# Optimization experiments

Hardware: AMD Instinct MI355X
Metric: run time of the kernel (lower is better)

Reference implementation:

```python
import jax, jax.numpy as jnp
import numpy as np
from jax import lax

E = 192      # hidden size
NH = 6       # attention heads
L = 6        # mixer blocks (permutation length)
CO = 256     # merging output channels
KH, KW = 7, 11   # locality window
LOCAL = (False, False, True, True, True, True)
B, H, W = 64, 8, 64


def skew(x, pad_value):
    # shift every row one step right, turning columns into diagonals (torch skew)
    rest = x.shape[:-2]
    Hd, Wd = x.shape[-2], x.shape[-1]
    x = jnp.pad(x, [(0, 0)] * (x.ndim - 1) + [(0, Hd)], constant_values=pad_value)
    x = x.reshape(*rest, -1)[..., : Hd * (Hd + Wd - 1)]
    x = x.reshape(*rest, Hd, Hd + Wd - 1)
    end = (Hd + Wd - 1) - (Wd // 2) + (Wd % 2 - 1)
    return x[..., Wd // 2 : end]


def make_mask(h, w, kh, kw):
    # boolean [h*w, h*w]; True inside the local window (torch: True = NOT allowed)
    m = jnp.ones((h, w, kh, kw), dtype=bool)
    m = m.transpose(0, 2, 1, 3)        # [h, kh, w, kw]
    m = skew(m, 0)                     # [h, kh, w, w]
    m = m.transpose(2, 3, 0, 1)        # [w, w, h, kh]
    m = skew(m, 0)                     # [w, w, h, h]
    m = m.transpose(2, 0, 3, 1)        # [h, w, h, w]
    return m.reshape(h * w, h * w)


def layernorm(x, g, b, eps=1e-5):
    mu = jnp.mean(x, axis=-1, keepdims=True)
    var = jnp.mean((x - mu) ** 2, axis=-1, keepdims=True)
    return (x - mu) / jnp.sqrt(var + eps) * g + b


def mha(x, mask, wi, bi, wo, bo, nh):
    # torch nn.MultiheadAttention (batch_first, self-attn, inference)
    b, s, e = x.shape
    hd = e // nh
    qkv = x @ wi.T + bi                                   # [b, s, 3e]
    q, k, v = jnp.split(qkv, 3, axis=-1)
    to_heads = lambda t: t.reshape(b, s, nh, hd).transpose(0, 2, 1, 3)
    q, k, v = to_heads(q), to_heads(k), to_heads(v)
    scores = jnp.einsum('bhqd,bhkd->bhqk', q, k) / jnp.sqrt(jnp.asarray(hd, x.dtype))
    if mask is not None:
        scores = jnp.where(mask, -jnp.inf, scores)
    attn = jax.nn.softmax(scores, axis=-1)
    out = jnp.einsum('bhqk,bhkd->bhqd', attn, v)
    out = out.transpose(0, 2, 1, 3).reshape(b, s, e)
    return out @ wo.T + bo


def mixer_block(x, mask, wi, bi, wo, bo, g1, b1, g2, b2, wm1, bm1, wm2, bm2):
    x = layernorm(x, g1, b1)
    x = mha(x, mask, wi, bi, wo, bo, NH) + x
    x = layernorm(x, g2, b2)
    h = jax.nn.relu(x @ wm1.T + bm1)
    return h @ wm2.T + bm2 + x


def fvtr_stage(image, in_w, in_b, out_w, out_b, ln1_g, ln1_b, ln2_g, ln2_b,
               w1, b1, w2, b2, conv_w, conv_b, mln_g, mln_b):
    bsz, c, h, w = image.shape
    x = jnp.swapaxes(image, -1, -3).reshape(bsz, w * h, c)   # [B, W*H, C]
    mask = make_mask(h, w, KH, KW)
    for i, loc in enumerate(LOCAL):
        x = mixer_block(x, mask if loc else None,
                        in_w[i], in_b[i], out_w[i], out_b[i],
                        ln1_g[i], ln1_b[i], ln2_g[i], ln2_b[i],
                        w1[i], b1[i], w2[i], b2[i])
    x = jnp.swapaxes(x.reshape(bsz, w, h, c), -1, -3)        # [B, C, H, W]
    # MergingBlock: conv (3,1) stride (2,1) pad (1,0) + channel LayerNorm
    y = lax.conv_general_dilated(x, conv_w, window_strides=(2, 1),
                                 padding=((1, 1), (0, 0)),
                                 dimension_numbers=('NCHW', 'OIHW', 'NCHW'))
    y = y + conv_b[None, :, None, None]
    y = jnp.moveaxis(y, 1, -1)
    y = layernorm(y, mln_g, mln_b)
    return jnp.moveaxis(y, -1, 1)


def setup_inputs() -> dict:
    key = jax.random.key(0)
    ks = jax.random.split(key, 8)
    s = 0.02
    return {
        'image': jax.random.normal(ks[0], (B, E, H, W), jnp.float32),
        'in_w':  s * jax.random.normal(ks[1], (L, 3 * E, E), jnp.float32),
        'in_b':  jnp.zeros((L, 3 * E), jnp.float32),
        'out_w': s * jax.random.normal(ks[2], (L, E, E), jnp.float32),
        'out_b': jnp.zeros((L, E), jnp.float32),
        'ln1_g': jnp.ones((L, E), jnp.float32),
        'ln1_b': jnp.zeros((L, E), jnp.float32),
        'ln2_g': jnp.ones((L, E), jnp.float32),
        'ln2_b': jnp.zeros((L, E), jnp.float32),
        'w1':    s * jax.random.normal(ks[3], (L, 4 * E, E), jnp.float32),
        'b1':    jnp.zeros((L, 4 * E), jnp.float32),
        'w2':    s * jax.random.normal(ks[4], (L, E, 4 * E), jnp.float32),
        'b2':    jnp.zeros((L, E), jnp.float32),
        'conv_w': s * jax.random.normal(ks[5], (CO, E, 3, 1), jnp.float32),
        'conv_b': jnp.zeros((CO,), jnp.float32),
        'mln_g': jnp.ones((CO,), jnp.float32),
        'mln_b': jnp.zeros((CO,), jnp.float32),
    }


def reference(image, in_w, in_b, out_w, out_b, ln1_g, ln1_b, ln2_g, ln2_b,
              w1, b1, w2, b2, conv_w, conv_b, mln_g, mln_b):
    return fvtr_stage(image, in_w, in_b, out_w, out_b, ln1_g, ln1_b, ln2_g, ln2_b,
                      w1, b1, w2, b2, conv_w, conv_b, mln_g, mln_b)
```

## Files before the change

kernel.cpp:

```cpp
#include <hip/hip_runtime.h>
#include <hip/hip_bf16.h>
#include <math.h>

#define Bn   64
#define Ssz  512
#define Ed   192
#define NHd  6
#define HDd  32
#define Ld   6
#define COd  256
#define Himg 8
#define Wimg 64
#define Mrows (Bn*Ssz)

typedef unsigned int  uint;
typedef unsigned short ushort;
using short8 = __attribute__((ext_vector_type(8))) short;
using f32x4  = __attribute__((ext_vector_type(4))) float;

__device__ inline ushort f2b(float f) {
    uint u = __builtin_bit_cast(uint, f);
    u = (u + 0x7FFFu + ((u >> 16) & 1u)) >> 16;
    return (ushort)u;
}

__device__ __forceinline__ float fexp2(float x) {
#if __has_builtin(__builtin_amdgcn_exp2f)
    return __builtin_amdgcn_exp2f(x);
#else
    return exp2f(x);
#endif
}

__device__ __forceinline__ uint cvt_pk_bf16(float a, float b) {
    uint r;
    asm("v_cvt_pk_bf16_f32 %0, %1, %2" : "=v"(r) : "v"(a), "v"(b));
    return r;
}

__device__ __forceinline__ void gload16(const ushort* g, ushort* l, int lane) {
#if __has_builtin(__builtin_amdgcn_global_load_lds)
    __builtin_amdgcn_global_load_lds(
        (const __attribute__((address_space(1))) uint*)g,
        (__attribute__((address_space(3))) uint*)l, 16, 0, 0);
#else
    *(uint4*)(l + (size_t)lane * 8) = *(const uint4*)g;
#endif
}

__global__ __launch_bounds__(256) void cvt_weights(const float* __restrict__ in_w,
                                                   const float* __restrict__ out_w,
                                                   const float* __restrict__ w1,
                                                   const float* __restrict__ w2,
                                                   const float* __restrict__ convw,
                                                   ushort* __restrict__ Wb) {
    int t = blockIdx.x * 256 + threadIdx.x;
    if (t >= 2801664) return;
    float v;
    if (t < 663552)        v = in_w[t];
    else if (t < 884736)   v = out_w[t - 663552];
    else if (t < 1769472)  v = w1[t - 884736];
    else if (t < 2654208)  v = w2[t - 1769472];
    else {
        int u = t - 2654208;
        int co = u / 576, rem = u % 576;
        int kh = rem / Ed, c = rem % Ed;
        v = convw[((size_t)co * Ed + c) * 3 + kh];
    }
    Wb[t] = f2b(v);
}

__global__ __launch_bounds__(256) void reshape_ln(const float* __restrict__ img,
                                                  const float* __restrict__ g,
                                                  const float* __restrict__ bb,
                                                  float* __restrict__ outf,
                                                  ushort* __restrict__ outb) {
    __shared__ float lds[Ed * 65];
    const int b = blockIdx.x >> 3, h = blockIdx.x & 7;
    const int tid = threadIdx.x;
    const float* src = img + ((size_t)b * Ed * Himg + h) * Wimg;
    #pragma unroll
    for (int i = 0; i < 48; ++i) {
        int idx = i * 256 + tid;
        int c = idx >> 6, w = idx & 63;
        lds[c * 65 + w] = src[(size_t)c * 512 + w];
    }
    __syncthreads();

    const int w = tid >> 2, q = tid & 3;
    float vals[48];
    float s = 0.f;
    #pragma unroll
    for (int j = 0; j < 48; ++j) {
        vals[j] = lds[(q * 48 + j) * 65 + w];
        s += vals[j];
    }
    s += __shfl_xor(s, 1); s += __shfl_xor(s, 2);
    float mu = s * (1.f / 192.f);
    float qv = 0.f;
    #pragma unroll
    for (int j = 0; j < 48; ++j) { float d = vals[j] - mu; qv += d * d; }
    qv += __shfl_xor(qv, 1); qv += __shfl_xor(qv, 2);
    float rstd = rsqrtf(qv * (1.f / 192.f) + 1e-5f);

    size_t row = (size_t)b * Ssz + w * Himg + h;
    float*  of = outf + row * Ed + q * 48;
    ushort* ob = outb + row * Ed + q * 48;
    const float* gg = g + q * 48;
    const float* bv = bb + q * 48;
    #pragma unroll
    for (int j = 0; j < 48; ++j) {
        float y = (vals[j] - mu) * rstd * gg[j] + bv[j];
        of[j] = y;
        ob[j] = f2b(y);
    }
}

template<int RELU, int RESID, int OBF, int VOUT>
__global__ __launch_bounds__(256) void gemm_mfma(
    const ushort* __restrict__ A, const ushort* __restrict__ Wt,
    const float* __restrict__ bias, const float* __restrict__ resid,
    float* __restrict__ C, ushort* __restrict__ Cb,
    ushort* __restrict__ qpout, ushort* __restrict__ kpout,
    ushort* __restrict__ vtout,
    int M, int N, int K)
{
    __shared__ __align__(16) ushort As[12288];
    __shared__ __align__(16) ushort Bs[6144];
    const int tid  = threadIdx.x;
    const int lane = tid & 63;
    const int wave = tid >> 6;
    const int wr = wave >> 1, wc = wave & 1;
    const int bm = blockIdx.x * 128;
    const int bn = blockIdx.y * 64;

    const ushort* Ag[6]; ushort* Al[6];
    #pragma unroll
    for (int i = 0; i < 6; ++i) {
        int fa = 4 * i + wave;
        int msub = fa / 3, ksub = fa % 3;
        int m = msub * 16 + (lane & 15);
        int k = ksub * 32 + ((lane >> 4) << 3);
        Ag[i] = A + (size_t)(bm + m) * K + k;
        Al[i] = As + fa * 512;
    }
    const ushort* Bg[3]; ushort* Bl[3];
    #pragma unroll
    for (int i = 0; i < 3; ++i) {
        int fb = 4 * i + wave;
        int nsub = fb / 3, ksub = fb % 3;
        int n = nsub * 16 + (lane & 15);
        int k = ksub * 32 + ((lane >> 4) << 3);
        Bg[i] = Wt + (size_t)(bn + n) * K + k;
        Bl[i] = Bs + fb * 512;
    }

    f32x4 acc[4][2];
    #pragma unroll
    for (int i = 0; i < 4; ++i)
        #pragma unroll
        for (int j = 0; j < 2; ++j) acc[i][j] = (f32x4){0.f, 0.f, 0.f, 0.f};

    for (int k0 = 0; k0 < K; k0 += 96) {
        #pragma unroll
        for (int i = 0; i < 6; ++i) gload16(Ag[i] + k0, Al[i], lane);
        #pragma unroll
        for (int i = 0; i < 3; ++i) gload16(Bg[i] + k0, Bl[i], lane);
        __syncthreads();
        #pragma unroll
        for (int ksub = 0; ksub < 3; ++ksub) {
            short8 af[4], bf[2];
            #pragma unroll
            for (int ms = 0; ms < 4; ++ms)
                af[ms] = *(const short8*)(As + (((wr*4+ms)*3 + ksub) * 64 + lane) * 8);
            #pragma unroll
            for (int ns = 0; ns < 2; ++ns)
                bf[ns] = *(const short8*)(Bs + (((wc*2+ns)*3 + ksub) * 64 + lane) * 8);
            #pragma unroll
            for (int ms = 0; ms < 4; ++ms)
                #pragma unroll
                for (int ns = 0; ns < 2; ++ns)
                    acc[ms][ns] = __builtin_amdgcn_mfma_f32_16x16x32_bf16(
                        af[ms], bf[ns], acc[ms][ns], 0, 0, 0);
        }
        __syncthreads();
    }

    int q = lane >> 4, colL = lane & 15;
    #pragma unroll
    for (int ms = 0; ms < 4; ++ms) {
        #pragma unroll
        for (int ns = 0; ns < 2; ++ns) {
            int row0 = bm + (wr*4 + ms) * 16 + q * 4;
            int col  = bn + (wc*2 + ns) * 16 + colL;
            float bvv = bias[col];
            float v[4];
            #pragma unroll
            for (int r = 0; r < 4; ++r) {
                v[r] = acc[ms][ns][r] + bvv;
                if (RELU) v[r] = fmaxf(v[r], 0.f);
                if (RESID) v[r] += resid[(size_t)(row0 + r) * N + col];
            }
            if (VOUT) {
                int bidx = row0 >> 9, srow = row0 & 511;
                if (col >= 384) {
                    int hh = (col - 384) >> 5, dd = (col - 384) & 31;
                    int sr = srow ^ ((((srow >> 2) ^ (srow >> 3)) & 1) * 12);
                    ushort4 pv;
                    pv.x = f2b(v[0]); pv.y = f2b(v[1]); pv.z = f2b(v[2]); pv.w = f2b(v[3]);
                    *(ushort4*)(vtout + (((size_t)(bidx * NHd + hh) * 32 + dd) << 9) + sr) = pv;
                } else {
                    ushort* dst = (col < 192) ? qpout : kpout;
                    int cc = (col < 192) ? col : col - 192;
                    if (col < 192) {
                        const float c2 = 0.2550547270628364f;
                        #pragma unroll
                        for (int r = 0; r < 4; ++r) v[r] *= c2;
                    }
                    int hh = cc >> 5, dd = cc & 31;
                    ushort* p = dst + ((size_t)(bidx * NHd + hh) << 14) + (size_t)srow * 32 + dd;
                    p[0]  = f2b(v[0]); p[32] = f2b(v[1]);
                    p[64] = f2b(v[2]); p[96] = f2b(v[3]);
                }
            } else {
                #pragma unroll
                for (int r = 0; r < 4; ++r) {
                    if (OBF) Cb[(size_t)(row0 + r) * N + col] = f2b(v[r]);
                    else     C [(size_t)(row0 + r) * N + col] = v[r];
                }
            }
        }
    }
}

template<int KIT, int MODE>
__global__ __launch_bounds__(256) void gemm_ln(
    const ushort* __restrict__ A, const ushort* __restrict__ Wt,
    const float* __restrict__ bias, const float* __restrict__ resid,
    const float* __restrict__ lng, const float* __restrict__ lnb,
    float* __restrict__ outf, ushort* __restrict__ outb,
    ushort* __restrict__ a2out)
{
    __shared__ __align__(16) ushort As[4096];
    __shared__ __align__(16) ushort Bs[12288];
    const int K = KIT * 64;
    const int lane = threadIdx.x & 63;
    const int wave = threadIdx.x >> 6;
    const int g = lane >> 4, ql = lane & 15;
    const int bm = blockIdx.x * 64;

    const ushort* Gp[8]; ushort* Lp[8];
    #pragma unroll
    for (int i = 0; i < 8; ++i) {
        int f = 4 * i + wave;
        if (f < 8) {
            int msub = f >> 1, ksub = f & 1;
            Gp[i] = A + (size_t)(bm + msub * 16 + ql) * K + ksub * 32 + g * 8;
            Lp[i] = As + f * 512;
        } else {
            int fb = f - 8, nsub = fb >> 1, ksub = fb & 1;
            Gp[i] = Wt + (size_t)(nsub * 16 + ql) * K + ksub * 32 + g * 8;
            Lp[i] = Bs + fb * 512;
        }
    }

    f32x4 acc[12];
    #pragma unroll
    for (int i = 0; i < 12; ++i) acc[i] = (f32x4){0.f, 0.f, 0.f, 0.f};

    for (int kc = 0; kc < KIT; ++kc) {
        #pragma unroll
        for (int i = 0; i < 8; ++i) gload16(Gp[i] + kc * 64, Lp[i], lane);
        __syncthreads();
        #pragma unroll
        for (int ksub = 0; ksub < 2; ++ksub) {
            short8 af = *(const short8*)(As + ((wave * 2 + ksub) * 64 + lane) * 8);
            #pragma unroll
            for (int ns = 0; ns < 12; ++ns) {
                short8 bf = *(const short8*)(Bs + ((ns * 2 + ksub) * 64 + lane) * 8);
                acc[ns] = __builtin_amdgcn_mfma_f32_16x16x32_bf16(af, bf, acc[ns], 0, 0, 0);
            }
        }
        __syncthreads();
    }

    float bi[12], gg[12], bb[12];
    #pragma unroll
    for (int ns = 0; ns < 12; ++ns) {
        int col = ns * 16 + ql;
        bi[ns] = bias[col];
        if (MODE == 1) { gg[ns] = lng[col]; bb[ns] = lnb[col]; }
    }
    #pragma unroll
    for (int r = 0; r < 4; ++r) {
        int row = bm + wave * 16 + g * 4 + r;
        float v[12];
        #pragma unroll
        for (int ns = 0; ns < 12; ++ns)
            v[ns] = acc[ns][r] + bi[ns] + resid[(size_t)row * Ed + ns * 16 + ql];
        if (MODE == 1) {
            float s = 0.f;
            #pragma unroll
            for (int ns = 0; ns < 12; ++ns) s += v[ns];
            s += __shfl_xor(s, 1); s += __shfl_xor(s, 2);
            s += __shfl_xor(s, 4); s += __shfl_xor(s, 8);
            float mu = s * (1.f / 192.f);
            float qv = 0.f;
            #pragma unroll
            for (int ns = 0; ns < 12; ++ns) { float d = v[ns] - mu; qv += d * d; }
            qv += __shfl_xor(qv, 1); qv += __shfl_xor(qv, 2);
            qv += __shfl_xor(qv, 4); qv += __shfl_xor(qv, 8);
            float rstd = rsqrtf(qv * (1.f / 192.f) + 1e-5f);
            #pragma unroll
            for (int ns = 0; ns < 12; ++ns) {
                float y = (v[ns] - mu) * rstd * gg[ns] + bb[ns];
                int col = ns * 16 + ql;
                outf[(size_t)row * Ed + col] = y;
                outb[(size_t)row * Ed + col] = f2b(y);
            }
        } else if (MODE == 2) {
            int bz = row >> 9, s = row & 511;
            int w = s >> 3, h = s & 7;
            #pragma unroll
            for (int ho = 0; ho < 4; ++ho) {
                int kh = h + 1 - 2 * ho;
                if (kh >= 0 && kh < 3) {
                    size_t r2 = ((size_t)((bz * 4 + ho) * 64 + w)) * 576 + kh * 192;
                    #pragma unroll
                    for (int ns = 0; ns < 12; ++ns)
                        a2out[r2 + ns * 16 + ql] = f2b(v[ns]);
                }
            }
            if (h == 0) {
                size_t r2 = ((size_t)(bz * 4 * 64 + w)) * 576;
                #pragma unroll
                for (int ns = 0; ns < 12; ++ns)
                    a2out[r2 + ns * 16 + ql] = 0;
            }
        } else {
            #pragma unroll
            for (int ns = 0; ns < 12; ++ns)
                outf[(size_t)row * Ed + ns * 16 + ql] = v[ns];
        }
    }
}

template<int USE_MASK>
__global__ __launch_bounds__(256) void attn_mfma(const ushort* __restrict__ qp,
                                                 const ushort* __restrict__ kp,
                                                 const ushort* __restrict__ vt,
                                                 ushort* __restrict__ att) {
    const int bh = blockIdx.x;
    const int b = bh / NHd, h = bh % NHd;
    const int wave = threadIdx.x >> 6, lane = threadIdx.x & 63;
    const int g = lane >> 4, ql = lane & 15;
    const int qb = blockIdx.y * 128 + wave * 32;

    const ushort* qbase = qp + ((size_t)bh << 14);
    const ushort* kbase = kp + ((size_t)bh << 14);
    const ushort* vbase = vt + ((size_t)bh << 14);
    short8 qf[2];
    #pragma unroll
    for (int t = 0; t < 2; ++t)
        qf[t] = *(const short8*)(qbase + (size_t)(qb + t * 16 + ql) * 32 + g * 8);

    short8 onesf;
    #pragma unroll
    for (int j = 0; j < 8; ++j) onesf[j] = (short)0x3F80;

    uint m0[2], m1[2]; int qh[2];
    if (USE_MASK) {
        #pragma unroll
        for (int t = 0; t < 2; ++t) {
            int qwt = ((qb + t * 16) & 63) + ql;
            qh[t] = (qb + t * 16) >> 6;
            uint a0 = 0, a1 = 0;
            #pragma unroll
            for (int i = 0; i < 8; ++i) {
                int keyl = (i >> 2) * 16 + 4 * g + (i & 3);
                int d0 = keyl - qwt;      d0 = d0 < 0 ? -d0 : d0;
                int d1 = keyl + 32 - qwt; d1 = d1 < 0 ? -d1 : d1;
                if (d0 <= 5) a0 |= (1u << i);
                if (d1 <= 5) a1 |= (1u << i);
            }
            m0[t] = a0; m1[t] = a1;
        }
    }

    f32x4 o0[2], o1[2], o2[2];
    #pragma unroll
    for (int t = 0; t < 2; ++t) {
        o0[t] = (f32x4){0.f,0.f,0.f,0.f};
        o1[t] = (f32x4){0.f,0.f,0.f,0.f};
        o2[t] = (f32x4){0.f,0.f,0.f,0.f};
    }
    const f32x4 z = {0.f,0.f,0.f,0.f};

    short8 kb_[3][2];
    short8 vb_[2][2];
    f32x4  st_[2][4];
    short8 pa[2];

    auto LK = [&](int kt, short8* d) {
        d[0] = *(const short8*)(kbase + (size_t)(kt * 32 + ql) * 32 + g * 8);
        d[1] = *(const short8*)(kbase + (size_t)(kt * 32 + 16 + ql) * 32 + g * 8);
    };
    auto LV = [&](int kt, short8* d) {
        d[0] = *(const short8*)(vbase + (size_t)ql * 512 + kt * 32 + 8 * g);
        d[1] = *(const short8*)(vbase + (size_t)(16 + ql) * 512 + kt * 32 + 8 * g);
    };
    auto S = [&](const short8* k, f32x4* st) {
        st[0] = __builtin_amdgcn_mfma_f32_16x16x32_bf16(k[0], qf[0], z, 0, 0, 0);
        st[1] = __builtin_amdgcn_mfma_f32_16x16x32_bf16(k[1], qf[0], z, 0, 0, 0);
        st[2] = __builtin_amdgcn_mfma_f32_16x16x32_bf16(k[0], qf[1], z, 0, 0, 0);
        st[3] = __builtin_amdgcn_mfma_f32_16x16x32_bf16(k[1], qf[1], z, 0, 0, 0);
    };
    auto F = [&](int kt, const f32x4* st) {
        #pragma unroll
        for (int t = 0; t < 2; ++t) {
            float p8[8];
            #pragma unroll
            for (int r = 0; r < 4; ++r) {
                p8[r]     = fexp2(st[t*2][r]);
                p8[4 + r] = fexp2(st[t*2+1][r]);
            }
            if (USE_MASK) {
                int dh = (kt >> 1) - qh[t]; dh = dh < 0 ? -dh : dh;
                if (dh <= 3) {
                    uint mm = (kt & 1) ? m1[t] : m0[t];
                    #pragma unroll
                    for (int i = 0; i < 8; ++i)
                        if ((mm >> i) & 1u) p8[i] = 0.f;
                }
            }
            uint Au = cvt_pk_bf16(p8[0], p8[1]);
            uint Bu = cvt_pk_bf16(p8[2], p8[3]);
            uint Cu = cvt_pk_bf16(p8[4], p8[5]);
            uint Du = cvt_pk_bf16(p8[6], p8[7]);
            asm("v_permlane32_swap_b32 %0, %1" : "+v"(Au), "+v"(Cu));
            asm("v_permlane32_swap_b32 %0, %1" : "+v"(Bu), "+v"(Du));
            union { uint u[4]; short8 s; } pk;
            pk.u[0] = Au; pk.u[1] = Bu; pk.u[2] = Cu; pk.u[3] = Du;
            pa[t] = pk.s;
        }
    };
    auto PV = [&](const short8* v) {
        #pragma unroll
        for (int t = 0; t < 2; ++t) {
            o0[t] = __builtin_amdgcn_mfma_f32_16x16x32_bf16(pa[t], v[0], o0[t], 0, 0, 0);
            o1[t] = __builtin_amdgcn_mfma_f32_16x16x32_bf16(pa[t], v[1], o1[t], 0, 0, 0);
            o2[t] = __builtin_amdgcn_mfma_f32_16x16x32_bf16(pa[t], onesf, o2[t], 0, 0, 0);
        }
    };

    LK(0, kb_[0]); LK(1, kb_[1]); LK(2, kb_[2]);
    LV(0, vb_[0]); LV(1, vb_[1]);
    S(kb_[0], st_[0]);
    #pragma unroll
    for (int kt = 0; kt < 16; ++kt) {
        if (kt < 15) S(kb_[(kt + 1) % 3], st_[(kt + 1) & 1]);
        if (kt < 13) LK(kt + 3, kb_[kt % 3]);
        F(kt, st_[kt & 1]);
        __builtin_amdgcn_s_setprio(1);
        PV(vb_[kt & 1]);
        __builtin_amdgcn_s_setprio(0);
        if (kt < 14) LV(kt + 2, vb_[kt & 1]);
    }

    ushort* op = att + (size_t)b * Ssz * Ed + h * 32;
    #pragma unroll
    for (int t = 0; t < 2; ++t) {
        #pragma unroll
        for (int r = 0; r < 4; ++r) {
            float iv = 1.f / o2[t][r];
            int row = qb + t * 16 + 4 * g + r;
            op[(size_t)row * Ed + ql]      = f2b(o0[t][r] * iv);
            op[(size_t)row * Ed + 16 + ql] = f2b(o1[t][r] * iv);
        }
    }
}

__global__ __launch_bounds__(256) void ln_out_kernel(const float* __restrict__ C2,
                                                     const float* __restrict__ g,
                                                     const float* __restrict__ beta,
                                                     float* __restrict__ out) {
    __shared__ float lds[32 * 257];
    int w0 = blockIdx.x * 32, ho = blockIdx.y, b = blockIdx.z;
    int tid = threadIdx.x;
    size_t rbase = ((size_t)b * 4 + ho) * 64 + w0;

    for (int i = 0; i < 32; ++i)
        lds[i * 257 + tid] = C2[(rbase + i) * COd + tid];
    __syncthreads();

    int wv = tid >> 6, lane = tid & 63;
    for (int rr = 0; rr < 8; ++rr) {
        int i = wv * 8 + rr;
        float v0 = lds[i*257 + lane], v1 = lds[i*257 + lane + 64];
        float v2 = lds[i*257 + lane + 128], v3 = lds[i*257 + lane + 192];
        float s = v0 + v1 + v2 + v3;
        #pragma unroll
        for (int off = 32; off > 0; off >>= 1) s += __shfl_xor(s, off);
        float mu = s * (1.f / 256.f);
        float d0 = v0-mu, d1 = v1-mu, d2 = v2-mu, d3 = v3-mu;
        float qv = d0*d0 + d1*d1 + d2*d2 + d3*d3;
        #pragma unroll
        for (int off = 32; off > 0; off >>= 1) qv += __shfl_xor(qv, off);
        float rstd = rsqrtf(qv * (1.f / 256.f) + 1e-5f);
        lds[i*257 + lane]       = d0 * rstd * g[lane]       + beta[lane];
        lds[i*257 + lane + 64]  = d1 * rstd * g[lane + 64]  + beta[lane + 64];
        lds[i*257 + lane + 128] = d2 * rstd * g[lane + 128] + beta[lane + 128];
        lds[i*257 + lane + 192] = d3 * rstd * g[lane + 192] + beta[lane + 192];
    }
    __syncthreads();

    int w = tid & 31, half = tid >> 5;
    for (int j = 0; j < 32; ++j) {
        int co = half + j * 8;
        out[(((size_t)b * COd + co) * 4 + ho) * Wimg + w0 + w] = lds[w * 257 + co];
    }
}

extern "C" void kernel_launch(void* const* d_in, const int* in_sizes, int n_in,
                              void* d_out, int out_size, void* d_ws, size_t ws_size,
                              hipStream_t stream) {
    const float* image = (const float*)d_in[0];
    const float* in_w  = (const float*)d_in[1];
    const float* in_b  = (const float*)d_in[2];
    const float* out_w = (const float*)d_in[3];
    const float* out_b = (const float*)d_in[4];
    const float* ln1_g = (const float*)d_in[5];
    const float* ln1_b = (const float*)d_in[6];
    const float* ln2_g = (const float*)d_in[7];
    const float* ln2_b = (const float*)d_in[8];
    const float* w1    = (const float*)d_in[9];
    const float* b1    = (const float*)d_in[10];
    const float* w2    = (const float*)d_in[11];
    const float* b2    = (const float*)d_in[12];
    const float* convw = (const float*)d_in[13];
    const float* convb = (const float*)d_in[14];
    const float* mln_g = (const float*)d_in[15];
    const float* mln_b = (const float*)d_in[16];
    float* out = (float*)d_out;
    float* ws  = (float*)d_ws;

    float* F1   = ws;
    float* F2   = ws + 6291456;
    float* BIG  = ws + 12582912;
    ushort* QP   = (ushort*)BIG;
    ushort* KP   = (ushort*)(BIG + 3145728);
    ushort* VT   = (ushort*)(BIG + 6291456);
    ushort* Hb   = (ushort*)BIG;
    float*  C2   = BIG + 4718592;
    ushort* XNb  = (ushort*)(BIG + 12582912);
    ushort* A2b  = (ushort*)(ws + 25165824);
    ushort* ATTb = (ushort*)(ws + 28311552);
    ushort* Wb   = (ushort*)(ws + 31457280);

    ushort* in_wb  = Wb;
    ushort* out_wb = Wb + 663552;
    ushort* w1b    = Wb + 884736;
    ushort* w2b    = Wb + 1769472;
    ushort* cwb    = Wb + 2654208;

    cvt_weights<<<(2801664 + 255) / 256, 256, 0, stream>>>(
        in_w, out_w, w1, w2, convw, Wb);

    reshape_ln<<<Bn * Himg, 256, 0, stream>>>(image, ln1_g, ln1_b, F1, XNb);

    for (int i = 0; i < Ld; ++i) {
        gemm_mfma<0,0,1,1><<<dim3(Mrows/128, 9), 256, 0, stream>>>(
            XNb, in_wb + (size_t)i * 3*Ed*Ed, in_b + i * 3*Ed,
            nullptr, nullptr, nullptr, QP, KP, VT, Mrows, 3*Ed, Ed);
        if (i >= 2) attn_mfma<1><<<dim3(Bn * NHd, 4), 256, 0, stream>>>(QP, KP, VT, ATTb);
        else        attn_mfma<0><<<dim3(Bn * NHd, 4), 256, 0, stream>>>(QP, KP, VT, ATTb);
        gemm_ln<3,1><<<Mrows/64, 256, 0, stream>>>(
            ATTb, out_wb + (size_t)i * Ed*Ed, out_b + i*Ed,
            F1, ln2_g + i*Ed, ln2_b + i*Ed, F2, XNb, nullptr);
        gemm_mfma<1,0,1,0><<<dim3(Mrows/128, 12), 256, 0, stream>>>(
            XNb, w1b + (size_t)i * 4*Ed*Ed, b1 + i * 4*Ed,
            nullptr, nullptr, Hb, nullptr, nullptr, nullptr, Mrows, 4*Ed, Ed);
        if (i < Ld - 1) {
            gemm_ln<12,1><<<Mrows/64, 256, 0, stream>>>(
                Hb, w2b + (size_t)i * 4*Ed*Ed, b2 + i*Ed,
                F2, ln1_g + (i+1)*Ed, ln1_b + (i+1)*Ed, F1, XNb, nullptr);
        } else {
            gemm_ln<12,2><<<Mrows/64, 256, 0, stream>>>(
                Hb, w2b + (size_t)i * 4*Ed*Ed, b2 + i*Ed,
                F2, nullptr, nullptr, nullptr, nullptr, A2b);
        }
    }

    gemm_mfma<0,0,0,0><<<dim3(16384/128, 4), 256, 0, stream>>>(
        A2b, cwb, convb, nullptr, C2, nullptr, nullptr, nullptr, nullptr,
        16384, COd, 576);
    ln_out_kernel<<<dim3(2, 4, Bn), 256, 0, stream>>>(C2, mln_g, mln_b, out);
}
```

Baseline: 1.043 ms.

## Fuse MLP up and down projections into one kernel keeping hidden in registers

Replaces the separate W1 GEMM plus the W2 GEMM+LayerNorm with a single fused_mlp kernel. Each wave computes 32-wide chunks of the ReLU hidden activations via MFMA, repacks them into A-operand layout with permlane32 swaps, and feeds them straight into the second GEMM accumulators. This removes the bf16 hidden tensor round-trip through global memory and one launch per layer, and W2 columns are pre-permuted during weight conversion to match the register layout. In exchange, weights are read directly from global memory per wave without LDS staging, and register pressure rises sharply.

```diff
diff --git a/kernel.cpp b/kernel.cpp
--- a/kernel.cpp
+++ b/kernel.cpp
@@ -60,8 +60,12 @@
     if (t < 663552)        v = in_w[t];
     else if (t < 884736)   v = out_w[t - 663552];
     else if (t < 1769472)  v = w1[t - 884736];
-    else if (t < 2654208)  v = w2[t - 1769472];
-    else {
+    else if (t < 2654208) {
+        int u = t - 1769472;
+        int k = u % 768;
+        int ks = k ^ ((((k >> 2) ^ (k >> 3)) & 1) * 12);
+        v = w2[u - k + ks];
+    } else {
         int u = t - 2654208;
         int co = u / 576, rem = u % 576;
         int kh = rem / Ed, c = rem % Ed;
@@ -233,13 +237,12 @@
     }
 }
 
-template<int KIT, int MODE>
+template<int KIT>
 __global__ __launch_bounds__(256) void gemm_ln(
     const ushort* __restrict__ A, const ushort* __restrict__ Wt,
     const float* __restrict__ bias, const float* __restrict__ resid,
     const float* __restrict__ lng, const float* __restrict__ lnb,
-    float* __restrict__ outf, ushort* __restrict__ outb,
-    ushort* __restrict__ a2out)
+    float* __restrict__ outf, ushort* __restrict__ outb)
 {
     __shared__ __align__(16) ushort As[4096];
     __shared__ __align__(16) ushort Bs[12288];
@@ -289,7 +292,7 @@
     for (int ns = 0; ns < 12; ++ns) {
         int col = ns * 16 + ql;
         bi[ns] = bias[col];
-        if (MODE == 1) { gg[ns] = lng[col]; bb[ns] = lnb[col]; }
+        gg[ns] = lng[col]; bb[ns] = lnb[col];
     }
     #pragma unroll
     for (int r = 0; r < 4; ++r) {
@@ -298,6 +301,112 @@
         #pragma unroll
         for (int ns = 0; ns < 12; ++ns)
             v[ns] = acc[ns][r] + bi[ns] + resid[(size_t)row * Ed + ns * 16 + ql];
+        float s = 0.f;
+        #pragma unroll
+        for (int ns = 0; ns < 12; ++ns) s += v[ns];
+        s += __shfl_xor(s, 1); s += __shfl_xor(s, 2);
+        s += __shfl_xor(s, 4); s += __shfl_xor(s, 8);
+        float mu = s * (1.f / 192.f);
+        float qv = 0.f;
+        #pragma unroll
+        for (int ns = 0; ns < 12; ++ns) { float d = v[ns] - mu; qv += d * d; }
+        qv += __shfl_xor(qv, 1); qv += __shfl_xor(qv, 2);
+        qv += __shfl_xor(qv, 4); qv += __shfl_xor(qv, 8);
+        float rstd = rsqrtf(qv * (1.f / 192.f) + 1e-5f);
+        #pragma unroll
+        for (int ns = 0; ns < 12; ++ns) {
+            float y = (v[ns] - mu) * rstd * gg[ns] + bb[ns];
+            int col = ns * 16 + ql;
+            outf[(size_t)row * Ed + col] = y;
+            outb[(size_t)row * Ed + col] = f2b(y);
+        }
+    }
+}
+
+template<int MODE>
+__global__ __launch_bounds__(256) void fused_mlp(
+    const ushort* __restrict__ X, const ushort* __restrict__ W1,
+    const float* __restrict__ b1, const ushort* __restrict__ W2k,
+    const float* __restrict__ b2, const float* __restrict__ resid,
+    const float* __restrict__ lng, const float* __restrict__ lnb,
+    float* __restrict__ outf, ushort* __restrict__ outb,
+    ushort* __restrict__ a2out)
+{
+    const int lane = threadIdx.x & 63;
+    const int wave = threadIdx.x >> 6;
+    const int g = lane >> 4, ql = lane & 15;
+    const int bm = blockIdx.x * 64;
+    const int row16 = bm + wave * 16;
+    const f32x4 z = {0.f,0.f,0.f,0.f};
+
+    short8 xf[6];
+    #pragma unroll
+    for (int ks = 0; ks < 6; ++ks)
+        xf[ks] = *(const short8*)(X + (size_t)(row16 + ql) * Ed + ks * 32 + g * 8);
+
+    f32x4 yacc[12];
+    #pragma unroll
+    for (int i = 0; i < 12; ++i) yacc[i] = z;
+
+    #pragma unroll
+    for (int c = 0; c < 24; ++c) {
+        short8 w2f[12];
+        #pragma unroll
+        for (int n2 = 0; n2 < 12; ++n2)
+            w2f[n2] = *(const short8*)(W2k + (size_t)(n2 * 16 + ql) * 768 + c * 32 + g * 8);
+        short8 w1f0[6], w1f1[6];
+        #pragma unroll
+        for (int ks = 0; ks < 6; ++ks) {
+            w1f0[ks] = *(const short8*)(W1 + (size_t)(c * 32 + ql) * Ed + ks * 32 + g * 8);
+            w1f1[ks] = *(const short8*)(W1 + (size_t)(c * 32 + 16 + ql) * Ed + ks * 32 + g * 8);
+        }
+        float4 bA = *(const float4*)(b1 + c * 32 + 4 * g);
+        float4 bB = *(const float4*)(b1 + c * 32 + 16 + 4 * g);
+
+        f32x4 st0 = z, st1 = z;
+        #pragma unroll
+        for (int ks = 0; ks < 6; ++ks) {
+            st0 = __builtin_amdgcn_mfma_f32_16x16x32_bf16(w1f0[ks], xf[ks], st0, 0, 0, 0);
+            st1 = __builtin_amdgcn_mfma_f32_16x16x32_bf16(w1f1[ks], xf[ks], st1, 0, 0, 0);
+        }
+        float p8[8];
+        p8[0] = fmaxf(st0[0] + bA.x, 0.f);
+        p8[1] = fmaxf(st0[1] + bA.y, 0.f);
+        p8[2] = fmaxf(st0[2] + bA.z, 0.f);
+        p8[3] = fmaxf(st0[3] + bA.w, 0.f);
+        p8[4] = fmaxf(st1[0] + bB.x, 0.f);
+        p8[5] = fmaxf(st1[1] + bB.y, 0.f);
+        p8[6] = fmaxf(st1[2] + bB.z, 0.f);
+        p8[7] = fmaxf(st1[3] + bB.w, 0.f);
+        uint Au = cvt_pk_bf16(p8[0], p8[1]);
+        uint Bu = cvt_pk_bf16(p8[2], p8[3]);
+        uint Cu = cvt_pk_bf16(p8[4], p8[5]);
+        uint Du = cvt_pk_bf16(p8[6], p8[7]);
+        asm("v_permlane32_swap_b32 %0, %1" : "+v"(Au), "+v"(Cu));
+        asm("v_permlane32_swap_b32 %0, %1" : "+v"(Bu), "+v"(Du));
+        union { uint u[4]; short8 s; } pk;
+        pk.u[0] = Au; pk.u[1] = Bu; pk.u[2] = Cu; pk.u[3] = Du;
+        short8 pa = pk.s;
+
+        #pragma unroll
+        for (int n2 = 0; n2 < 12; ++n2)
+            yacc[n2] = __builtin_amdgcn_mfma_f32_16x16x32_bf16(pa, w2f[n2], yacc[n2], 0, 0, 0);
+    }
+
+    float bi[12], gg[12], bb[12];
+    #pragma unroll
+    for (int ns = 0; ns < 12; ++ns) {
+        int col = ns * 16 + ql;
+        bi[ns] = b2[col];
+        if (MODE == 1) { gg[ns] = lng[col]; bb[ns] = lnb[col]; }
+    }
+    #pragma unroll
+    for (int r = 0; r < 4; ++r) {
+        int row = row16 + g * 4 + r;
+        float v[12];
+        #pragma unroll
+        for (int ns = 0; ns < 12; ++ns)
+            v[ns] = yacc[ns][r] + bi[ns] + resid[(size_t)row * Ed + ns * 16 + ql];
         if (MODE == 1) {
             float s = 0.f;
             #pragma unroll
@@ -318,7 +427,7 @@
                 outf[(size_t)row * Ed + col] = y;
                 outb[(size_t)row * Ed + col] = f2b(y);
             }
-        } else if (MODE == 2) {
+        } else {
             int bz = row >> 9, s = row & 511;
             int w = s >> 3, h = s & 7;
             #pragma unroll
@@ -337,10 +446,6 @@
                 for (int ns = 0; ns < 12; ++ns)
                     a2out[r2 + ns * 16 + ql] = 0;
             }
-        } else {
-            #pragma unroll
-            for (int ns = 0; ns < 12; ++ns)
-                outf[(size_t)row * Ed + ns * 16 + ql] = v[ns];
         }
     }
 }
@@ -550,7 +655,6 @@
     ushort* QP   = (ushort*)BIG;
     ushort* KP   = (ushort*)(BIG + 3145728);
     ushort* VT   = (ushort*)(BIG + 6291456);
-    ushort* Hb   = (ushort*)BIG;
     float*  C2   = BIG + 4718592;
     ushort* XNb  = (ushort*)(BIG + 12582912);
     ushort* A2b  = (ushort*)(ws + 25165824);
@@ -574,20 +678,19 @@
             nullptr, nullptr, nullptr, QP, KP, VT, Mrows, 3*Ed, Ed);
         if (i >= 2) attn_mfma<1><<<dim3(Bn * NHd, 4), 256, 0, stream>>>(QP, KP, VT, ATTb);
         else        attn_mfma<0><<<dim3(Bn * NHd, 4), 256, 0, stream>>>(QP, KP, VT, ATTb);
-        gemm_ln<3,1><<<Mrows/64, 256, 0, stream>>>(
+        gemm_ln<3><<<Mrows/64, 256, 0, stream>>>(
             ATTb, out_wb + (size_t)i * Ed*Ed, out_b + i*Ed,
-            F1, ln2_g + i*Ed, ln2_b + i*Ed, F2, XNb, nullptr);
-        gemm_mfma<1,0,1,0><<<dim3(Mrows/128, 12), 256, 0, stream>>>(
-            XNb, w1b + (size_t)i * 4*Ed*Ed, b1 + i * 4*Ed,
-            nullptr, nullptr, Hb, nullptr, nullptr, nullptr, Mrows, 4*Ed, Ed);
+            F1, ln2_g + i*Ed, ln2_b + i*Ed, F2, XNb);
         if (i < Ld - 1) {
-            gemm_ln<12,1><<<Mrows/64, 256, 0, stream>>>(
-                Hb, w2b + (size_t)i * 4*Ed*Ed, b2 + i*Ed,
-                F2, ln1_g + (i+1)*Ed, ln1_b + (i+1)*Ed, F1, XNb, nullptr);
+            fused_mlp<1><<<Mrows/64, 256, 0, stream>>>(
+                XNb, w1b + (size_t)i * 4*Ed*Ed, b1 + i * 4*Ed,
+                w2b + (size_t)i * 4*Ed*Ed, b2 + i*Ed, F2,
+                ln1_g + (i+1)*Ed, ln1_b + (i+1)*Ed, F1, XNb, nullptr);
         } else {
-            gemm_ln<12,2><<<Mrows/64, 256, 0, stream>>>(
-                Hb, w2b + (size_t)i * 4*Ed*Ed, b2 + i*Ed,
-                F2, nullptr, nullptr, nullptr, nullptr, A2b);
+            fused_mlp<2><<<Mrows/64, 256, 0, stream>>>(
+                XNb, w1b + (size_t)i * 4*Ed*Ed, b1 + i * 4*Ed,
+                w2b + (size_t)i * 4*Ed*Ed, b2 + i*Ed, F2,
+                nullptr, nullptr, nullptr, nullptr, A2b);
         }
     }
 
```

Result: slower. 1.537 ms (+47.4%).
